# Performance work log

Measured on AMD Instinct MI355X. Metric: run time of the kernel, lower is better.

Reference implementation:

```python
import jax, jax.numpy as jnp
import numpy as np

NUM_TASKS = 150
ACT_DIM = 4
ENC_DIM = 256
EMB_DIM = 32
HEAD_HID = 128
B, H, W = 256, 128, 128


def _conv(x, w, b):
    # x: NCHW, w: OIHW, stride 2, padding 1 (torch Conv2d semantics)
    y = jax.lax.conv_general_dilated(x, w, window_strides=(2, 2),
                                     padding=((1, 1), (1, 1)),
                                     dimension_numbers=('NCHW', 'OIHW', 'NCHW'))
    return y + b[None, :, None, None]


def setup_inputs() -> dict:
    key = jax.random.key(0)
    ks = iter(jax.random.split(key, 32))
    s = 0.05
    d = {
        'images': jax.random.normal(next(ks), (B, 3, H, W), jnp.float32),
        'proprioception': jax.random.normal(next(ks), (B, 7), jnp.float32),
        'task_ids': jax.random.randint(next(ks), (B,), 0, NUM_TASKS, jnp.int32),
        # vision encoder convs (OIHW)
        'c1_w': jax.random.normal(next(ks), (64, 3, 3, 3), jnp.float32) * s,
        'c1_b': jnp.zeros((64,), jnp.float32),
        'c2_w': jax.random.normal(next(ks), (128, 64, 3, 3), jnp.float32) * s,
        'c2_b': jnp.zeros((128,), jnp.float32),
        'c3_w': jax.random.normal(next(ks), (256, 128, 3, 3), jnp.float32) * s,
        'c3_b': jnp.zeros((256,), jnp.float32),
        # proprioception encoder (weights stored as [in, out])
        'p1_w': jax.random.normal(next(ks), (7, 64), jnp.float32) * s,
        'p1_b': jnp.zeros((64,), jnp.float32),
        'p2_w': jax.random.normal(next(ks), (64, 64), jnp.float32) * s,
        'p2_b': jnp.zeros((64,), jnp.float32),
        # shared-encoder fusion MLP (320 -> 256 -> 256)
        'f1_w': jax.random.normal(next(ks), (256 + 64, ENC_DIM), jnp.float32) * s,
        'f1_b': jnp.zeros((ENC_DIM,), jnp.float32),
        'f2_w': jax.random.normal(next(ks), (ENC_DIM, ENC_DIM), jnp.float32) * s,
        'f2_b': jnp.zeros((ENC_DIM,), jnp.float32),
        # task embedding table
        'task_emb': jax.random.normal(next(ks), (NUM_TASKS, EMB_DIM), jnp.float32) * s,
        # policy-level fusion (288 -> 256), dropout is identity at inference
        'g_w': jax.random.normal(next(ks), (ENC_DIM + EMB_DIM, ENC_DIM), jnp.float32) * s,
        'g_b': jnp.zeros((ENC_DIM,), jnp.float32),
        # stacked task-specific heads [num_tasks, in, out]
        'h1_w': jax.random.normal(next(ks), (NUM_TASKS, ENC_DIM, HEAD_HID), jnp.float32) * s,
        'h1_b': jnp.zeros((NUM_TASKS, HEAD_HID), jnp.float32),
        'h2_w': jax.random.normal(next(ks), (NUM_TASKS, HEAD_HID, HEAD_HID), jnp.float32) * s,
        'h2_b': jnp.zeros((NUM_TASKS, HEAD_HID), jnp.float32),
        'h3_w': jax.random.normal(next(ks), (NUM_TASKS, HEAD_HID, ACT_DIM), jnp.float32) * s,
        'h3_b': jnp.zeros((NUM_TASKS, ACT_DIM), jnp.float32),
    }
    return d


def reference(images, proprioception, task_ids,
              c1_w, c1_b, c2_w, c2_b, c3_w, c3_b,
              p1_w, p1_b, p2_w, p2_b,
              f1_w, f1_b, f2_w, f2_b,
              task_emb, g_w, g_b,
              h1_w, h1_b, h2_w, h2_b, h3_w, h3_b):
    relu = jax.nn.relu
    # vision encoder: 3 strided convs + global avg pool (AdaptiveAvgPool2d(1,1))
    v = relu(_conv(images, c1_w, c1_b))
    v = relu(_conv(v, c2_w, c2_b))
    v = relu(_conv(v, c3_w, c3_b))
    v = jnp.mean(v, axis=(2, 3))                      # [B, 256]
    # proprioception encoder (no final ReLU)
    p = relu(proprioception @ p1_w + p1_b) @ p2_w + p2_b  # [B, 64]
    # shared fusion
    f = relu(jnp.concatenate([v, p], axis=1) @ f1_w + f1_b)
    f = relu(f @ f2_w + f2_b)                         # [B, 256]
    # task embedding + policy fusion (dropout = identity in eval)
    e = task_emb[task_ids]                            # [B, 32]
    z = relu(jnp.concatenate([f, e], axis=1) @ g_w + g_b)  # [B, 256]
    # routed task heads: gather per-sample expert params, batched matmuls
    a = relu(jnp.einsum('bd,bdh->bh', z, h1_w[task_ids]) + h1_b[task_ids])
    a = relu(jnp.einsum('bd,bdh->bh', a, h2_w[task_ids]) + h2_b[task_ids])
    a = jnp.einsum('bd,bdh->bh', a, h3_w[task_ids]) + h3_b[task_ids]  # [B, 4]
    return a
```

## Files before the change

### kernel.cpp

```cpp
#include <hip/hip_runtime.h>
#include <hip/hip_bf16.h>

#define DIV_UP(a,b) (((a)+(b)-1)/(b))

typedef __attribute__((ext_vector_type(8))) short short8;
typedef __attribute__((ext_vector_type(4))) float f32x4;

__device__ __forceinline__ ushort bf16_bits(float x) {
    return __builtin_bit_cast(ushort, __float2bfloat16(x));
}

__device__ __forceinline__ void gload_lds16(const ushort* g, ushort* l) {
    __builtin_amdgcn_global_load_lds(
        (const __attribute__((address_space(1))) void*)g,
        (__attribute__((address_space(3))) void*)l, 16, 0, 0);
}

__global__ __launch_bounds__(256) void halo_zero_kernel(
    uint4* __restrict__ act1, uint4* __restrict__ act2,
    float4* __restrict__ vbuf) {
    const int b = blockIdx.x, tid = threadIdx.x;
    const uint4 z = {0u, 0u, 0u, 0u};
    uint4* a1 = act1 + (size_t)b * 33800;
    for (int i = tid; i < 520; i += 256) a1[i] = z;
    for (int i = tid; i < 512; i += 256) {
        int r = (i >> 3) + 1;
        a1[r * 520 + (i & 7)] = z;
    }
    uint4* a2 = act2 + (size_t)b * 17424;
    for (int i = tid; i < 528; i += 256) a2[i] = z;
    for (int i = tid; i < 512; i += 256) {
        int r = (i >> 4) + 1;
        a2[r * 528 + (i & 15)] = z;
    }
    int idx = b * 256 + tid;
    float4 zf = {0.f, 0.f, 0.f, 0.f};
    if (idx < 16384) vbuf[idx] = zf;
}

__global__ void repack_w1_kernel(const float* __restrict__ src,
                                 __hip_bfloat16* __restrict__ dst) {
    int t = blockIdx.x * blockDim.x + threadIdx.x;
    if (t >= 2048) return;
    int k  = t & 31;
    int oc = t >> 5;
    dst[t] = (k < 27) ? __float2bfloat16(src[oc * 27 + k])
                      : __float2bfloat16(0.f);
}

__global__ void repack_w_kernel(const float* __restrict__ src,
                                __hip_bfloat16* __restrict__ dst, int O, int C) {
    int t = blockIdx.x * blockDim.x + threadIdx.x;
    if (t >= O * C * 9) return;
    int e   = t & 7;
    int r   = t >> 3;
    int n   = r % O;
    int q   = r / O;
    int SEG = C >> 3;
    int sg  = q % SEG;
    int tap = q / SEG;
    dst[t] = __float2bfloat16(src[(n * C + sg * 8 + e) * 9 + tap]);
}

__global__ __launch_bounds__(256) void conv1_mfma_kernel(
    const float* __restrict__ in,
    const __hip_bfloat16* __restrict__ wB,
    const float* __restrict__ bias,
    __hip_bfloat16* __restrict__ out) {
    const int tid  = threadIdx.x;
    const int lane = tid & 63;
    const int wv   = tid >> 6;
    const int l15  = lane & 15;
    const int quad = lane >> 4;
    const int tile = blockIdx.x;
    const int b    = blockIdx.y;
    const int oh0  = tile << 2;

    __shared__ __align__(16) char smem[36864];
    float*  sx = (float*)smem;
    ushort* Al = (ushort*)(smem + 14256);
    ushort* Cs = (ushort*)smem;

    const float* ip  = in + (size_t)b * 3 * 128 * 128;
    const int    ih0 = 2 * oh0 - 1;
    for (int e = tid; e < 3510; e += 256) {
        int c   = e / 1170;
        int rem = e - c * 1170;
        int r   = rem / 130;
        int col = rem - r * 130;
        int ih  = ih0 + r;
        int iw  = col - 1;
        bool ok = ((unsigned)ih < 128u) && ((unsigned)iw < 128u);
        sx[(c * 9 + r) * 132 + col] = ok ? ip[c * 16384 + ih * 128 + iw] : 0.f;
    }
    __syncthreads();

    {
        const int px = tid, ohl = px >> 6, ow = px & 63;
        union { uint4 u4[4]; ushort us[32]; } rowv;
#pragma unroll
        for (int k = 0; k < 27; ++k) {
            const int c = k / 9, rm = k - c * 9, kh = rm / 3, kw = rm - kh * 3;
            rowv.us[k] = bf16_bits(sx[(c * 9 + 2 * ohl + kh) * 132 + 2 * ow + kw]);
        }
#pragma unroll
        for (int k = 27; k < 32; ++k) rowv.us[k] = 0;
#pragma unroll
        for (int q = 0; q < 4; ++q)
            *(uint4*)(Al + px * 32 + (((q ^ (px >> 1)) & 3) << 3)) = rowv.u4[q];
    }
    __syncthreads();

    short8 af[4], bf[4];
#pragma unroll
    for (int i = 0; i < 4; ++i)
        af[i] = __builtin_bit_cast(short8,
            *(const uint4*)(wB + ((i * 16 + l15) * 32 + quad * 8)));
#pragma unroll
    for (int j = 0; j < 4; ++j) {
        int p = wv * 64 + j * 16 + l15;
        bf[j] = __builtin_bit_cast(short8,
            *(const uint4*)(Al + p * 32 + (((quad ^ (p >> 1)) & 3) << 3)));
    }
    f32x4 acc[4][4];
#pragma unroll
    for (int i = 0; i < 4; ++i)
#pragma unroll
        for (int j = 0; j < 4; ++j)
            acc[i][j] = __builtin_amdgcn_mfma_f32_16x16x32_bf16(
                af[i], bf[j], (f32x4){0.f, 0.f, 0.f, 0.f}, 0, 0, 0);

    float4 bv[4];
#pragma unroll
    for (int i = 0; i < 4; ++i)
        bv[i] = *(const float4*)(bias + i * 16 + quad * 4);

    __syncthreads();

#pragma unroll
    for (int j = 0; j < 4; ++j) {
        const int px = wv * 64 + j * 16 + l15;
#pragma unroll
        for (int i = 0; i < 4; ++i) {
            union { uint2 u2; ushort us[4]; } pk;
#pragma unroll
            for (int r = 0; r < 4; ++r)
                pk.us[r] = bf16_bits(
                    fmaxf(acc[i][j][r] + ((const float*)&bv[i])[r], 0.f));
            *(uint2*)(Cs + px * 72 + i * 16 + quad * 4) = pk.u2;
        }
    }
    __syncthreads();

    __hip_bfloat16* ob = out + (((size_t)b * 65 + oh0 + 1) * 65 + 1) * 64;
#pragma unroll
    for (int it = 0; it < 8; ++it) {
        int g   = it * 256 + tid;
        int px  = g >> 3, cq = g & 7;
        uint4 v = *(const uint4*)(Cs + px * 72 + cq * 8);
        int ohl = px >> 6, ow = px & 63;
        *(uint4*)(ob + ((size_t)ohl * 65 + ow) * 64 + cq * 8) = v;
    }
}

__global__ __launch_bounds__(256, 2) void conv2_gemm_kernel(
    const __hip_bfloat16* __restrict__ act,
    const __hip_bfloat16* __restrict__ wtB,
    const float* __restrict__ bias,
    __hip_bfloat16* __restrict__ out) {
    const int tid  = threadIdx.x;
    const int lane = tid & 63;
    const int w    = tid >> 6;
    const int l15  = lane & 15;
    const int quad = lane >> 4;
    const int per  = gridDim.x >> 3;
    const int Mt   = (blockIdx.x & 7) * per + (blockIdx.x >> 3);
    const int bimg = Mt >> 3;
    const int oh0  = (Mt & 7) << 2;

    __shared__ __align__(16) char smem[77824];
    ushort* As = (ushort*)smem;
    ushort* Cs = (ushort*)smem;

    f32x4 acc[4][4];
#pragma unroll
    for (int i = 0; i < 4; ++i)
#pragma unroll
        for (int j = 0; j < 4; ++j) acc[i][j] = (f32x4){0.f, 0.f, 0.f, 0.f};

    const int wm = (w & 1) << 6;
    const int wn = (w >> 1) << 6;
    const size_t abase = ((size_t)(bimg * 65 + 2 * oh0)) * 65 * 64;
    const ushort* ap = (const ushort*)act;

#pragma unroll
    for (int it = 0; it < 19; ++it) {
        int c  = (it << 8) + tid;
        int p  = c >> 3;
        int t  = c & 7;
        int h  = t >> 2;
        int ss = (t & 3) ^ ((p >> 1) & 3);
        gload_lds16(ap + abase + (size_t)p * 64 + h * 32 + ss * 8,
                    As + (size_t)c * 8);
    }
    __syncthreads();

    for (int h = 0; h < 2; ++h) {
#pragma unroll
        for (int tap = 0; tap < 9; ++tap) {
            const int kh = tap / 3, kw = tap - kh * 3;
            short8 af[4], bf[4];
#pragma unroll
            for (int i = 0; i < 4; ++i) {
                int ml = wm + i * 16 + l15;
                int p  = ((ml >> 5) * 2 + kh) * 65 + ((ml & 31) * 2 + kw);
                af[i] = __builtin_bit_cast(short8,
                    *(const uint4*)(As + p * 64 + h * 32 +
                                    (((quad ^ (p >> 1)) & 3) << 3)));
            }
#pragma unroll
            for (int j = 0; j < 4; ++j)
                bf[j] = __builtin_bit_cast(short8,
                    *(const uint4*)(wtB +
                        ((size_t)((tap * 8 + h * 4 + quad) * 128) +
                         wn + j * 16 + l15) * 8));
#pragma unroll
            for (int i = 0; i < 4; ++i)
#pragma unroll
                for (int j = 0; j < 4; ++j)
                    acc[i][j] = __builtin_amdgcn_mfma_f32_16x16x32_bf16(
                        af[i], bf[j], acc[i][j], 0, 0, 0);
        }
    }

    __syncthreads();
#pragma unroll
    for (int j = 0; j < 4; ++j) {
        int n = wn + j * 16 + l15;
        float bv = bias[n];
#pragma unroll
        for (int i = 0; i < 4; ++i)
#pragma unroll
            for (int r = 0; r < 4; ++r) {
                int ml = wm + i * 16 + quad * 4 + r;
                Cs[ml * 132 + n] = bf16_bits(fmaxf(acc[i][j][r] + bv, 0.f));
            }
    }
    __syncthreads();
#pragma unroll
    for (int q = 0; q < 16; ++q) {
        int c   = tid + 256 * q;
        int row = c >> 5;
        int off = c & 31;
        uint2 val = *(const uint2*)(Cs + row * 132 + off * 4);
        int m  = (Mt << 7) + row;
        int b  = m >> 10;
        int rr = m & 1023;
        int oh = rr >> 5;
        int ow = rr & 31;
        size_t pix = ((size_t)(b * 33 + oh + 1) * 33 + (ow + 1));
        *(uint2*)(out + pix * 128 + off * 4) = val;
    }
}

__global__ __launch_bounds__(256, 2) void conv3_gemm_pool_kernel(
    const __hip_bfloat16* __restrict__ act,
    const __hip_bfloat16* __restrict__ wtB,
    const float* __restrict__ bias,
    float* __restrict__ v ) {
    const int tid  = threadIdx.x;
    const int lane = tid & 63;
    const int w    = tid >> 6;
    const int l15  = lane & 15;
    const int quad = lane >> 4;
    const int per  = gridDim.x >> 3;
    const int Mt   = (blockIdx.x & 7) * per + (blockIdx.x >> 3);
    const int bimg = Mt >> 2;
    const int oh0  = (Mt & 3) << 2;

    __shared__ __align__(16) char smem[77824];
    ushort* As   = (ushort*)smem;
    float*  sred = (float*)smem;

    f32x4 acc[4][4];
#pragma unroll
    for (int i = 0; i < 4; ++i)
#pragma unroll
        for (int j = 0; j < 4; ++j) acc[i][j] = (f32x4){0.f, 0.f, 0.f, 0.f};

    const int wn = w << 6;
    const size_t abase = ((size_t)(bimg * 33 + 2 * oh0)) * 33 * 128;
    const ushort* ap = (const ushort*)act;

#pragma unroll
    for (int it = 0; it < 19; ++it) {
        int c  = (it << 8) + tid;
        int p  = c >> 4;
        int t  = c & 15;
        int h  = t >> 3;
        int ss = (t & 7) ^ ((p >> 1) & 7);
        gload_lds16(ap + abase + (size_t)p * 128 + h * 64 + ss * 8,
                    As + (size_t)c * 8);
    }
    __syncthreads();

    for (int h = 0; h < 2; ++h) {
#pragma unroll 1
        for (int tap = 0; tap < 9; ++tap) {
            const int kh = tap / 3, kw = tap - kh * 3;
#pragma unroll
            for (int ks = 0; ks < 2; ++ks) {
                short8 af[4], bf[4];
                const int sl = ks * 4 + quad;
#pragma unroll
                for (int i = 0; i < 4; ++i) {
                    int p = (i * 2 + kh) * 33 + l15 * 2 + kw;
                    af[i] = __builtin_bit_cast(short8,
                        *(const uint4*)(As + p * 128 + h * 64 +
                                        (((sl ^ (p >> 1)) & 7) << 3)));
                }
#pragma unroll
                for (int j = 0; j < 4; ++j)
                    bf[j] = __builtin_bit_cast(short8,
                        *(const uint4*)(wtB +
                            ((size_t)((tap * 16 + h * 8 + sl) * 256) +
                             wn + j * 16 + l15) * 8));
#pragma unroll
                for (int i = 0; i < 4; ++i)
#pragma unroll
                    for (int j = 0; j < 4; ++j)
                        acc[i][j] = __builtin_amdgcn_mfma_f32_16x16x32_bf16(
                            af[i], bf[j], acc[i][j], 0, 0, 0);
            }
        }
    }

    float s4[4];
#pragma unroll
    for (int j = 0; j < 4; ++j) {
        float bv = bias[wn + j * 16 + l15];
        float s = 0.f;
#pragma unroll
        for (int i = 0; i < 4; ++i)
#pragma unroll
            for (int r = 0; r < 4; ++r)
                s += fmaxf(acc[i][j][r] + bv, 0.f);
        s += __shfl_xor(s, 16, 64);
        s += __shfl_xor(s, 32, 64);
        s4[j] = s;
    }
    __syncthreads();
    if (quad == 0) {
#pragma unroll
        for (int j = 0; j < 4; ++j) sred[wn + j * 16 + l15] = s4[j];
    }
    __syncthreads();
    atomicAdd(v + (size_t)bimg * 256 + tid, sred[tid] * (1.f / 256.f));
}

template<int N, int K, int S, bool RELU>
__device__ __forceinline__ void gemv_stage(const float* __restrict__ w,
                                           const float* __restrict__ bias,
                                           const float* in, float* outv,
                                           float4* red4, int tid) {
    constexpr int G = N / 4;
    constexpr int CHK = K / S;
    static_assert(G * S == 256 && CHK * S == K, "stage shape");
    const int g = tid % G, s = tid / G;
    const float4* wp = (const float4*)w;
    float4 a; a.x = a.y = a.z = a.w = 0.f;
    const int k0 = s * CHK;
#pragma unroll 8
    for (int i = 0; i < CHK; ++i) {
        float x = in[k0 + i];
        float4 wv = wp[(size_t)(k0 + i) * G + g];
        a.x = fmaf(x, wv.x, a.x);
        a.y = fmaf(x, wv.y, a.y);
        a.z = fmaf(x, wv.z, a.z);
        a.w = fmaf(x, wv.w, a.w);
    }
    red4[tid] = a;
    __syncthreads();
    if (tid < N) {
        int gg = tid >> 2, e = tid & 3;
        float vv = bias[tid];
#pragma unroll
        for (int ss = 0; ss < S; ++ss) {
            const float* rp = (const float*)(red4 + ss * G + gg);
            vv += rp[e];
        }
        if (RELU) vv = fmaxf(vv, 0.f);
        outv[tid] = vv;
    }
    __syncthreads();
}

__global__ __launch_bounds__(256) void tail_kernel(
    const float* __restrict__ prop, const int* __restrict__ task_ids,
    const float* __restrict__ p1_w, const float* __restrict__ p1_b,
    const float* __restrict__ p2_w, const float* __restrict__ p2_b,
    const float* __restrict__ v,
    const float* __restrict__ f1_w, const float* __restrict__ f1_b,
    const float* __restrict__ f2_w, const float* __restrict__ f2_b,
    const float* __restrict__ task_emb,
    const float* __restrict__ g_w, const float* __restrict__ g_b,
    const float* __restrict__ h1_w, const float* __restrict__ h1_b,
    const float* __restrict__ h2_w, const float* __restrict__ h2_b,
    const float* __restrict__ h3_w, const float* __restrict__ h3_b,
    float* __restrict__ out) {
    const int b   = blockIdx.x;
    const int tid = threadIdx.x;
    const int t   = task_ids[b];
    __shared__ float sa[320];
    __shared__ float sb[288];
    __shared__ float sph[64];
    __shared__ float4 red4[256];

    sa[tid] = (tid < 256) ? v[(size_t)b * 256 + tid] : 0.f;
    if (tid < 64) {
        float h = p1_b[tid];
#pragma unroll
        for (int k = 0; k < 7; ++k) h = fmaf(prop[b * 7 + k], p1_w[k * 64 + tid], h);
        sph[tid] = fmaxf(h, 0.f);
    }
    __syncthreads();
    gemv_stage<64, 64, 16, false>(p2_w, p2_b, sph, sa + 256, red4, tid);
    gemv_stage<256, 320, 4, true>(f1_w, f1_b, sa, sb, red4, tid);
    gemv_stage<256, 256, 4, true>(f2_w, f2_b, sb, sa, red4, tid);
    if (tid < 32) sa[256 + tid] = task_emb[t * 32 + tid];
    __syncthreads();
    gemv_stage<256, 288, 4, true>(g_w, g_b, sa, sb, red4, tid);
    gemv_stage<128, 256, 8, true>(h1_w + (size_t)t * 32768, h1_b + t * 128,
                                  sb, sa, red4, tid);
    gemv_stage<128, 128, 8, true>(h2_w + (size_t)t * 16384, h2_b + t * 128,
                                  sa, sb, red4, tid);
    if (tid < 128) {
        float4 wv = ((const float4*)(h3_w + (size_t)t * 512))[tid];
        float x = sb[tid];
        float r0 = x * wv.x, r1 = x * wv.y, r2 = x * wv.z, r3 = x * wv.w;
#pragma unroll
        for (int off = 1; off < 64; off <<= 1) {
            r0 += __shfl_xor(r0, off, 64);
            r1 += __shfl_xor(r1, off, 64);
            r2 += __shfl_xor(r2, off, 64);
            r3 += __shfl_xor(r3, off, 64);
        }
        if ((tid & 63) == 0) {
            float4 rv; rv.x = r0; rv.y = r1; rv.z = r2; rv.w = r3;
            red4[tid >> 6] = rv;
        }
    }
    __syncthreads();
    if (tid < 4) {
        const float* ra = (const float*)(red4 + 0);
        const float* rb = (const float*)(red4 + 1);
        out[b * 4 + tid] = ra[tid] + rb[tid] + h3_b[t * 4 + tid];
    }
}

extern "C" void kernel_launch(void* const* d_in, const int* in_sizes, int n_in,
                              void* d_out, int out_size, void* d_ws, size_t ws_size,
                              hipStream_t stream) {
    (void)in_sizes; (void)n_in; (void)out_size;
    const float* images   = (const float*)d_in[0];
    const float* prop     = (const float*)d_in[1];
    const int*   task_ids = (const int*)d_in[2];
    const float* c1_w = (const float*)d_in[3];
    const float* c1_b = (const float*)d_in[4];
    const float* c2_w = (const float*)d_in[5];
    const float* c2_b = (const float*)d_in[6];
    const float* c3_w = (const float*)d_in[7];
    const float* c3_b = (const float*)d_in[8];
    const float* p1_w = (const float*)d_in[9];
    const float* p1_b = (const float*)d_in[10];
    const float* p2_w = (const float*)d_in[11];
    const float* p2_b = (const float*)d_in[12];
    const float* f1_w = (const float*)d_in[13];
    const float* f1_b = (const float*)d_in[14];
    const float* f2_w = (const float*)d_in[15];
    const float* f2_b = (const float*)d_in[16];
    const float* temb = (const float*)d_in[17];
    const float* g_w  = (const float*)d_in[18];
    const float* g_b  = (const float*)d_in[19];
    const float* h1_w = (const float*)d_in[20];
    const float* h1_b = (const float*)d_in[21];
    const float* h2_w = (const float*)d_in[22];
    const float* h2_b = (const float*)d_in[23];
    const float* h3_w = (const float*)d_in[24];
    const float* h3_b = (const float*)d_in[25];
    float* out = (float*)d_out;

    const size_t per_img = (size_t)65 * 65 * 64 * 2 + (size_t)33 * 33 * 128 * 2;
    const size_t fixed   = (size_t)256 * 256 * 4 + 1728 * 4 +
                           (size_t)73728 * 2 + (size_t)294912 * 2 + 4096;
    int CHI = 64;
    if (ws_size >= fixed + per_img * 256) CHI = 256;
    else if (ws_size >= fixed + per_img * 128) CHI = 128;

    char* ws = (char*)d_ws;
    size_t off = 0;
    auto alloc = [&](size_t bytes) {
        void* p = ws + off;
        off += (bytes + 255) & ~(size_t)255;
        return p;
    };
    __hip_bfloat16* act1 = (__hip_bfloat16*)alloc((size_t)CHI * 65 * 65 * 64 * 2);
    __hip_bfloat16* act2 = (__hip_bfloat16*)alloc((size_t)CHI * 33 * 33 * 128 * 2);
    float*          vbuf = (float*)alloc((size_t)256 * 256 * 4);
    __hip_bfloat16* w1b  = (__hip_bfloat16*)alloc((size_t)2048 * 2);
    __hip_bfloat16* w2t  = (__hip_bfloat16*)alloc((size_t)73728 * 2);
    __hip_bfloat16* w3t  = (__hip_bfloat16*)alloc((size_t)294912 * 2);

    halo_zero_kernel<<<dim3(CHI), 256, 0, stream>>>(
        (uint4*)act1, (uint4*)act2, (float4*)vbuf);
    repack_w1_kernel<<<8, 256, 0, stream>>>(c1_w, w1b);
    repack_w_kernel<<<DIV_UP(73728, 256), 256, 0, stream>>>(c2_w, w2t, 128, 64);
    repack_w_kernel<<<DIV_UP(294912, 256), 256, 0, stream>>>(c3_w, w3t, 256, 128);

    for (int c0 = 0; c0 < 256; c0 += CHI) {
        const float* img_c = images + (size_t)c0 * 3 * 128 * 128;
        conv1_mfma_kernel<<<dim3(16, CHI), dim3(256), 0, stream>>>(
            img_c, w1b, c1_b, act1);
        conv2_gemm_kernel<<<dim3(CHI * 8), 256, 0, stream>>>(
            act1, w2t, c2_b, act2);
        conv3_gemm_pool_kernel<<<dim3(CHI * 4), 256, 0, stream>>>(
            act2, w3t, c3_b, vbuf + (size_t)c0 * 256);
    }
    tail_kernel<<<256, 256, 0, stream>>>(prop, task_ids, p1_w, p1_b, p2_w, p2_b,
                                         vbuf, f1_w, f1_b, f2_w, f2_b, temb,
                                         g_w, g_b, h1_w, h1_b, h2_w, h2_b,
                                         h3_w, h3_b, out);
}
```

Measured before the change: 352.8 us.

## Load conv1 im2col taps directly from global and store output without LDS staging

Conv1 now skips staging the fp32 input halo tile in shared memory. Each thread gathers its 27 im2col taps directly from global memory, relying on the cache for overlap between neighbouring pixels. The epilogue also drops the LDS transpose and writes bias+ReLU results straight to global as 8-byte stores. This cuts shared memory use and two barriers, which may raise occupancy, but global reads are strided (stride-2 columns) and output stores are smaller and less coalesced.

Measured after the change: 372.8 us. +5.7%, slower.

```diff
diff --git a/kernel.cpp b/kernel.cpp
--- a/kernel.cpp
+++ b/kernel.cpp
@@ -76,46 +76,56 @@
     const int b    = blockIdx.y;
     const int oh0  = tile << 2;
 
-    __shared__ __align__(16) char smem[36864];
-    float*  sx = (float*)smem;
-    ushort* Al = (ushort*)(smem + 14256);
-    ushort* Cs = (ushort*)smem;
-
-    const float* ip  = in + (size_t)b * 3 * 128 * 128;
-    const int    ih0 = 2 * oh0 - 1;
-    for (int e = tid; e < 3510; e += 256) {
-        int c   = e / 1170;
-        int rem = e - c * 1170;
-        int r   = rem / 130;
-        int col = rem - r * 130;
-        int ih  = ih0 + r;
-        int iw  = col - 1;
-        bool ok = ((unsigned)ih < 128u) && ((unsigned)iw < 128u);
-        sx[(c * 9 + r) * 132 + col] = ok ? ip[c * 16384 + ih * 128 + iw] : 0.f;
-    }
-    __syncthreads();
-
-    {
-        const int px = tid, ohl = px >> 6, ow = px & 63;
-        union { uint4 u4[4]; ushort us[32]; } rowv;
-#pragma unroll
-        for (int k = 0; k < 27; ++k) {
-            const int c = k / 9, rm = k - c * 9, kh = rm / 3, kw = rm - kh * 3;
-            rowv.us[k] = bf16_bits(sx[(c * 9 + 2 * ohl + kh) * 132 + 2 * ow + kw]);
-        }
-#pragma unroll
-        for (int k = 27; k < 32; ++k) rowv.us[k] = 0;
-#pragma unroll
-        for (int q = 0; q < 4; ++q)
-            *(uint4*)(Al + px * 32 + (((q ^ (px >> 1)) & 3) << 3)) = rowv.u4[q];
-    }
-    __syncthreads();
+    __shared__ __align__(16) ushort Al[256 * 32];
+
+    const int px  = tid;
+    const int ow  = px & 63;
+    const int ohg = oh0 + wv;
+
+    const float* ip = in + (size_t)b * 3 * 128 * 128;
+
+    int roff[3]; bool rv[3];
+#pragma unroll
+    for (int kh = 0; kh < 3; ++kh) {
+        int ih = 2 * ohg + kh - 1;
+        rv[kh]   = (ih >= 0);
+        roff[kh] = (ih >= 0 ? ih : 0) * 128;
+    }
+    int coff[3]; bool cv[3];
+#pragma unroll
+    for (int kw = 0; kw < 3; ++kw) {
+        int iw = 2 * ow + kw - 1;
+        cv[kw]   = (iw >= 0);
+        coff[kw] = (iw >= 0 ? iw : 0);
+    }
+
+    union { uint4 u4[4]; ushort us[32]; } rowv;
+#pragma unroll
+    for (int c = 0; c < 3; ++c) {
+        const float* pc = ip + c * 16384;
+#pragma unroll
+        for (int kh = 0; kh < 3; ++kh)
+#pragma unroll
+            for (int kw = 0; kw < 3; ++kw) {
+                float x = pc[roff[kh] + coff[kw]];
+                x = (rv[kh] && cv[kw]) ? x : 0.f;
+                rowv.us[c * 9 + kh * 3 + kw] = bf16_bits(x);
+            }
+    }
+#pragma unroll
+    for (int k = 27; k < 32; ++k) rowv.us[k] = 0;
+#pragma unroll
+    for (int q = 0; q < 4; ++q)
+        *(uint4*)(Al + px * 32 + (((q ^ (px >> 1)) & 3) << 3)) = rowv.u4[q];
 
     short8 af[4], bf[4];
 #pragma unroll
     for (int i = 0; i < 4; ++i)
         af[i] = __builtin_bit_cast(short8,
             *(const uint4*)(wB + ((i * 16 + l15) * 32 + quad * 8)));
+
+    __syncthreads();
+
 #pragma unroll
     for (int j = 0; j < 4; ++j) {
         int p = wv * 64 + j * 16 + l15;
@@ -135,11 +145,11 @@
     for (int i = 0; i < 4; ++i)
         bv[i] = *(const float4*)(bias + i * 16 + quad * 4);
 
-    __syncthreads();
-
+    __hip_bfloat16* ob = out + (((size_t)b * 65 + oh0 + 1) * 65 + 1) * 64;
 #pragma unroll
     for (int j = 0; j < 4; ++j) {
-        const int px = wv * 64 + j * 16 + l15;
+        const int oww = j * 16 + l15;
+        __hip_bfloat16* op = ob + ((size_t)(wv * 65) + oww) * 64 + quad * 4;
 #pragma unroll
         for (int i = 0; i < 4; ++i) {
             union { uint2 u2; ushort us[4]; } pk;
@@ -147,19 +157,8 @@
             for (int r = 0; r < 4; ++r)
                 pk.us[r] = bf16_bits(
                     fmaxf(acc[i][j][r] + ((const float*)&bv[i])[r], 0.f));
-            *(uint2*)(Cs + px * 72 + i * 16 + quad * 4) = pk.u2;
+            *(uint2*)(op + i * 16) = pk.u2;
         }
-    }
-    __syncthreads();
-
-    __hip_bfloat16* ob = out + (((size_t)b * 65 + oh0 + 1) * 65 + 1) * 64;
-#pragma unroll
-    for (int it = 0; it < 8; ++it) {
-        int g   = it * 256 + tid;
-        int px  = g >> 3, cq = g & 7;
-        uint4 v = *(const uint4*)(Cs + px * 72 + cq * 8);
-        int ohl = px >> 6, ow = px & 63;
-        *(uint4*)(ob + ((size_t)ohl * 65 + ow) * 64 + cq * 8) = v;
     }
 }
 
```
